# Performance work log

Hardware: AMD Instinct MI355X
Metric: run time of the kernel (lower is better)

Reference implementation:

```python
import jax, jax.numpy as jnp
import numpy as np

# dims: B=batch, S=src_len, H=hidden, E=char_embed, V=vocab, L=lstm layers
B, S, H, E, V, L = 512, 64, 1024, 256, 128, 2


def setup_inputs() -> dict:
    key = jax.random.key(0)
    ks = jax.random.split(key, 20)
    def n(k, shape, scale=0.05):
        return jax.random.normal(k, shape, dtype=jnp.float32) * scale
    return {
        "input_ids": jax.random.randint(ks[0], (B, 1), 0, V),
        "hidden": n(ks[1], (L, B, H), 1.0),
        "cell": n(ks[2], (L, B, H), 1.0),
        "encoder_outputs": n(ks[3], (B, S, H), 1.0),
        "emb": n(ks[4], (V, E)),          # nn.Embedding weight
        "U": n(ks[5], (H, H)),             # attention U (applied as x @ U)
        "W": n(ks[6], (H, H)),             # attention W
        "Vw": n(ks[7], (H, 1)),            # attention V -> scalar score
        "Wih0": n(ks[8], (4 * H, E + H)),  # LSTM layer0 input weights (i,f,g,o)
        "Whh0": n(ks[9], (4 * H, H)),
        "bih0": n(ks[10], (4 * H,)),
        "bhh0": n(ks[11], (4 * H,)),
        "Wih1": n(ks[12], (4 * H, H)),     # LSTM layer1
        "Whh1": n(ks[13], (4 * H, H)),
        "bih1": n(ks[14], (4 * H,)),
        "bhh1": n(ks[15], (4 * H,)),
        "out_w": n(ks[16], (V, H)),        # output nn.Linear weight (out,in)
        "out_b": n(ks[17], (V,)),
        "matrix": 0,
    }


def _lstm_step(x, h, c, Wih, Whh, bih, bhh):
    g = x @ Wih.T + h @ Whh.T + bih + bhh          # (B, 4H), torch gate order i,f,g,o
    i, f, gg, o = jnp.split(g, 4, axis=-1)
    c2 = jax.nn.sigmoid(f) * c + jax.nn.sigmoid(i) * jnp.tanh(gg)
    h2 = jax.nn.sigmoid(o) * jnp.tanh(c2)
    return h2, c2


def reference(input_ids, hidden, cell, encoder_outputs, emb, U, W, Vw,
              Wih0, Whh0, bih0, bhh0, Wih1, Whh1, bih1, bhh1,
              out_w, out_b, matrix):
    embedded = emb[input_ids]                                  # (B,1,E)
    t1 = jnp.einsum('bsh,hk->bsk', encoder_outputs, U)         # U(enc): (B,S,H)
    t2 = hidden[-1] @ W                                        # W(h_top): (B,H)
    e = jnp.tanh(t1 + t2[:, None, :]) @ Vw                     # scores: (B,S,1)
    a = jax.nn.softmax(e, axis=1)                              # attention weights over S
    ct = jnp.einsum('bso,bsh->boh', a, encoder_outputs)        # context: (B,1,H)
    x = jnp.concatenate([embedded, ct], axis=2)[:, 0, :]       # (B, E+H); dropout p=0 -> identity
    h0, c0 = _lstm_step(x, hidden[0], cell[0], Wih0, Whh0, bih0, bhh0)
    h1, c1 = _lstm_step(h0, hidden[1], cell[1], Wih1, Whh1, bih1, bhh1)
    out = (h1 @ out_w.T + out_b)[:, None, :]                   # (B,1,V)
    h_new = jnp.stack([h0, h1])
    c_new = jnp.stack([c0, c1])
    if matrix:
        return (a, out, h_new, c_new)
    return (out, h_new, c_new)
```

## Files before the change

kernel.cpp:

```cpp
#include <hip/hip_runtime.h>
#include <stdint.h>

#define BB 512
#define SS 64
#define HH 1024
#define EE 256
#define VV 128

typedef __attribute__((ext_vector_type(8))) short bf16x8;
typedef __attribute__((ext_vector_type(4))) float f32x4;
typedef __attribute__((ext_vector_type(8))) unsigned short u16x8;

constexpr size_t OFF_SCRATCH = 0;
constexpr size_t OFF_OUTW  = OFF_SCRATCH + 67108864UL;
constexpr size_t OFF_HID0  = OFF_OUTW  + 262144UL;
constexpr size_t OFF_HLAST = OFF_HID0  + 1048576UL;
constexpr size_t OFF_UT    = OFF_HLAST + 1048576UL;
constexpr size_t OFF_WT    = OFF_UT    + 2097152UL;
constexpr size_t OFF_T2    = OFF_WT    + 2097152UL;
constexpr size_t OFF_E     = OFF_T2    + 2097152UL;
constexpr size_t OFF_EMB   = OFF_E     + 131072UL;
constexpr size_t OFF_CT    = OFF_EMB   + 262144UL;
constexpr size_t OFF_G     = OFF_CT    + 1048576UL;
constexpr size_t OFF_H0B   = OFF_G     + 8388608UL;
constexpr size_t OFF_H1B   = OFF_H0B   + 1048576UL;

__device__ __forceinline__ unsigned short f2bf(float f) {
  unsigned int u = __float_as_uint(f);
  unsigned int r = (u + 0x7FFFu + ((u >> 16) & 1u)) >> 16;
  return (unsigned short)r;
}
__device__ __forceinline__ float bf2f(unsigned short h) {
  return __uint_as_float(((unsigned int)h) << 16);
}

__device__ __forceinline__ void gload_lds16(const void* g, void* l) {
  __builtin_amdgcn_global_load_lds(
      (const __attribute__((address_space(1))) unsigned int*)g,
      (__attribute__((address_space(3))) unsigned int*)l, 16, 0, 0);
}

__global__ __launch_bounds__(256) void cvt_small(const float* __restrict__ hid,
                                                 const float* __restrict__ outw,
                                                 char* __restrict__ ws) {
  int i = blockIdx.x * 256 + threadIdx.x;
  const float4* src;
  ushort4* dst;
  int j;
  if (i < 262144) { src = (const float4*)hid;  dst = (ushort4*)(ws + OFF_HID0); j = i; }
  else            { src = (const float4*)outw; dst = (ushort4*)(ws + OFF_OUTW); j = i - 262144; }
  float4 v = src[j];
  ushort4 o;
  o.x = f2bf(v.x); o.y = f2bf(v.y); o.z = f2bf(v.z); o.w = f2bf(v.w);
  dst[j] = o;
}

__global__ void transpose_cvt2(const float* __restrict__ U, const float* __restrict__ W,
                               char* __restrict__ ws) {
  __shared__ float tile[32][33];
  const float* in = blockIdx.z ? W : U;
  unsigned short* out = (unsigned short*)(ws + (blockIdx.z ? OFF_WT : OFF_UT));
  int bc = blockIdx.x * 32, br = blockIdx.y * 32;
  int tx = threadIdx.x & 31, ty = threadIdx.x >> 5;
#pragma unroll
  for (int i = 0; i < 32; i += 8)
    tile[ty + i][tx] = in[(long)(br + ty + i) * HH + bc + tx];
  __syncthreads();
#pragma unroll
  for (int i = 0; i < 32; i += 8)
    out[(long)(bc + ty + i) * HH + br + tx] = f2bf(tile[tx][ty + i]);
}

__global__ void build_xemb(const int* __restrict__ ids, const float* __restrict__ emb,
                           unsigned short* __restrict__ embb) {
  int t = blockIdx.x * 256 + threadIdx.x;
  int b = t >> 6, c4 = t & 63;
  float4 v = ((const float4*)(emb + (long)ids[b] * 256))[c4];
  ushort4 o;
  o.x = f2bf(v.x); o.y = f2bf(v.y); o.z = f2bf(v.z); o.w = f2bf(v.w);
  ((ushort4*)embb)[t] = o;
}

template <int BF32>
__global__ __launch_bounds__(256) void gemm_seg(
    const unsigned short* __restrict__ A0, int KA0,
    const unsigned short* __restrict__ A1, int KA1,
    const unsigned short* __restrict__ A2,
    const void* __restrict__ B0v, int KB0, const void* __restrict__ B1v,
    float* __restrict__ C0p, float* __restrict__ C1p, int N, int Ktot, int Khalf) {
  __shared__ alignas(128) unsigned short lA[128 * 64];
  __shared__ alignas(128) unsigned short lB[64 * 64];
  const int tid = threadIdx.x;
  const int lane = tid & 63, wid = tid >> 6;
  const int wr = wid >> 1, wc = wid & 1;
  const int fr = lane & 15, fg = lane >> 4;
  f32x4 acc[4][2] = {};
  const long rowA0 = (long)blockIdx.x * 128;
  const long rowB0 = (long)blockIdx.y * 64;
  const int ktb = blockIdx.z * Khalf;
  int kte = ktb + Khalf; if (kte > Ktot) kte = Ktot;
  float* C = blockIdx.z ? C1p : C0p;
  for (int kt = ktb; kt < kte; kt += 64) {
    const unsigned short* Ap; int ka, lda;
    if (kt < KA0)            { Ap = A0; ka = kt;             lda = KA0; }
    else if (kt < KA0 + KA1) { Ap = A1; ka = kt - KA0;       lda = KA1; }
    else                     { Ap = A2; ka = kt - KA0 - KA1; lda = 1024; }
    if constexpr (BF32) {
      const float* Bp; int kb, ldb;
      if (kt < KB0) { Bp = (const float*)B0v; kb = kt;       ldb = KB0; }
      else          { Bp = (const float*)B1v; kb = kt - KB0; ldb = 1024; }
      const int brow = tid >> 2, bkq = tid & 3;
      const f32x4* bs = (const f32x4*)(Bp + (rowB0 + brow) * (long)ldb + kb) + bkq * 4;
      f32x4 q0 = bs[0], q1 = bs[1], q2 = bs[2], q3 = bs[3];
#pragma unroll
      for (int j = 0; j < 4; ++j) {
        int c = j * 256 + tid;
        int r = c >> 3, cc = c & 7;
        int sc = cc ^ ((r >> 1) & 7);
        gload_lds16(Ap + (rowA0 + r) * (long)lda + ka + sc * 8, &lA[c * 8]);
      }
      const int bx = (brow >> 1) & 7;
      u16x8 w0, w1;
#pragma unroll
      for (int j = 0; j < 4; ++j) {
        w0[j] = f2bf(q0[j]); w0[4 + j] = f2bf(q1[j]);
        w1[j] = f2bf(q2[j]); w1[4 + j] = f2bf(q3[j]);
      }
      *(u16x8*)&lB[brow * 64 + (((bkq * 2) ^ bx) * 8)] = w0;
      *(u16x8*)&lB[brow * 64 + (((bkq * 2 + 1) ^ bx) * 8)] = w1;
    } else {
      const unsigned short* Bp; int kb, ldb;
      if (kt < KB0) { Bp = (const unsigned short*)B0v; kb = kt;       ldb = KB0; }
      else          { Bp = (const unsigned short*)B1v; kb = kt - KB0; ldb = 1024; }
#pragma unroll
      for (int j = 0; j < 4; ++j) {
        int c = j * 256 + tid;
        int r = c >> 3, cc = c & 7;
        int sc = cc ^ ((r >> 1) & 7);
        gload_lds16(Ap + (rowA0 + r) * (long)lda + ka + sc * 8, &lA[c * 8]);
      }
#pragma unroll
      for (int j = 0; j < 2; ++j) {
        int c = j * 256 + tid;
        int r = c >> 3, cc = c & 7;
        int sc = cc ^ ((r >> 1) & 7);
        gload_lds16(Bp + (rowB0 + r) * (long)ldb + kb + sc * 8, &lB[c * 8]);
      }
    }
    __syncthreads();
#pragma unroll
    for (int kk = 0; kk < 64; kk += 32) {
      bf16x8 af[4], bfv[2];
#pragma unroll
      for (int m = 0; m < 4; ++m) {
        int row = wr * 64 + m * 16 + fr;
        int ch = ((kk >> 3) + fg) ^ ((row >> 1) & 7);
        af[m] = *(const bf16x8*)&lA[row * 64 + ch * 8];
      }
#pragma unroll
      for (int n = 0; n < 2; ++n) {
        int row = wc * 32 + n * 16 + fr;
        int ch = ((kk >> 3) + fg) ^ ((row >> 1) & 7);
        bfv[n] = *(const bf16x8*)&lB[row * 64 + ch * 8];
      }
#pragma unroll
      for (int m = 0; m < 4; ++m)
#pragma unroll
        for (int n = 0; n < 2; ++n)
          acc[m][n] = __builtin_amdgcn_mfma_f32_16x16x32_bf16(af[m], bfv[n],
                                                              acc[m][n], 0, 0, 0);
    }
    __syncthreads();
  }
#pragma unroll
  for (int m = 0; m < 4; ++m)
#pragma unroll
    for (int n = 0; n < 2; ++n)
#pragma unroll
      for (int r = 0; r < 4; ++r) {
        long grow = rowA0 + wr * 64 + m * 16 + fg * 4 + r;
        long gcol = rowB0 + wc * 32 + n * 16 + fr;
        C[grow * N + gcol] = acc[m][n][r];
      }
}

__global__ __launch_bounds__(256) void gemm_outproj(
    const unsigned short* __restrict__ A, const unsigned short* __restrict__ Bt,
    float* __restrict__ C) {
  __shared__ alignas(128) unsigned short lA[128 * 64];
  __shared__ alignas(128) unsigned short lB[128 * 64];
  const int tid = threadIdx.x;
  const int lane = tid & 63, wid = tid >> 6;
  const int wr = wid >> 1, wc = wid & 1;
  const int fr = lane & 15, fg = lane >> 4;
  f32x4 acc[4][4] = {};
  const long rowA0 = (long)blockIdx.x * 128;
  const int k0 = blockIdx.y * 128;
  for (int kt = k0; kt < k0 + 128; kt += 64) {
#pragma unroll
    for (int j = 0; j < 4; ++j) {
      int c = j * 256 + tid;
      int r = c >> 3, cc = c & 7;
      gload_lds16(A + (rowA0 + r) * 1024 + kt + cc * 8, &lA[c * 8]);
    }
#pragma unroll
    for (int j = 0; j < 4; ++j) {
      int c = j * 256 + tid;
      int r = c >> 3, cc = c & 7;
      gload_lds16(Bt + (long)r * 1024 + kt + cc * 8, &lB[c * 8]);
    }
    __syncthreads();
#pragma unroll
    for (int kk = 0; kk < 64; kk += 32) {
      bf16x8 af[4], bfv[4];
#pragma unroll
      for (int m = 0; m < 4; ++m)
        af[m] = *(const bf16x8*)&lA[(wr * 64 + m * 16 + fr) * 64 + kk + fg * 8];
#pragma unroll
      for (int n = 0; n < 4; ++n)
        bfv[n] = *(const bf16x8*)&lB[(wc * 64 + n * 16 + fr) * 64 + kk + fg * 8];
#pragma unroll
      for (int m = 0; m < 4; ++m)
#pragma unroll
        for (int n = 0; n < 4; ++n)
          acc[m][n] = __builtin_amdgcn_mfma_f32_16x16x32_bf16(af[m], bfv[n],
                                                              acc[m][n], 0, 0, 0);
    }
    __syncthreads();
  }
#pragma unroll
  for (int m = 0; m < 4; ++m)
#pragma unroll
    for (int n = 0; n < 4; ++n)
#pragma unroll
      for (int r = 0; r < 4; ++r) {
        long grow = rowA0 + wr * 64 + m * 16 + fg * 4 + r;
        long gcol = wc * 64 + n * 16 + fr;
        atomicAdd(&C[grow * 128 + gcol], acc[m][n][r]);
      }
}

__global__ void init_out_bias(const float* __restrict__ ob, float* __restrict__ out) {
  int i = blockIdx.x * 256 + threadIdx.x;
  out[i] = ob[i & 127];
}

__global__ __launch_bounds__(512, 2) void gemm_score128(
    const float* __restrict__ Af, const unsigned short* __restrict__ Bt,
    const float* __restrict__ t2, const float* __restrict__ Vw,
    float* __restrict__ e) {
  extern __shared__ unsigned short smem[];
  const int tid = threadIdx.x;
  const int lane = tid & 63, wid = tid >> 6;
  const int wr = wid >> 2;
  const int wcc = wid & 3;
  const int fr = lane & 15, fg = lane >> 4;
  int flat = blockIdx.y * 4 + blockIdx.x;
  int swz = (flat & 7) * 128 + (flat >> 3);
  const long rowA0 = (long)(swz >> 2) * 128;
  const long rowB0 = (long)(swz & 3) * 256;

  f32x4 acc[4][4] = {};

  const int arow = tid >> 2, akq = tid & 3;
  const int akh = akq >> 1, ach = akq & 1;
  const float* ag = Af + (rowA0 + arow) * 1024 + akq * 16;
  const int awx = (arow >> 1) & 3;
  f32x4 areg[4];

  auto issueA = [&](int kt) {
    const f32x4* p = (const f32x4*)(ag + kt * 64);
#pragma unroll
    for (int j = 0; j < 4; ++j) areg[j] = p[j];
  };
  auto writeA = [&](int buf) {
    unsigned short* wb = smem + buf * 24576 + akh * 4096 + arow * 32;
#pragma unroll
    for (int w = 0; w < 2; ++w) {
      u16x8 o;
#pragma unroll
      for (int q = 0; q < 8; ++q) o[q] = f2bf(areg[w * 2 + (q >> 2)][q & 3]);
      *(u16x8*)(wb + (((ach * 2 + w) ^ awx) * 8)) = o;
    }
  };
  auto stageB = [&](int buf, int kt) {
#pragma unroll
    for (int kh = 0; kh < 2; ++kh) {
      unsigned short* dst = smem + buf * 24576 + 8192 + kh * 8192;
      int kb = kt * 64 + kh * 32;
#pragma unroll
      for (int j = 0; j < 2; ++j) {
        int c = j * 512 + tid;
        int row = c >> 2;
        int fgl = (c & 3) ^ ((row >> 1) & 3);
        gload_lds16(Bt + (rowB0 + row) * 1024L + kb + fgl * 8, dst + c * 8);
      }
    }
  };
  auto readA4 = [&](int buf, int kh, bf16x8* af) {
    const unsigned short* rg = smem + buf * 24576 + kh * 4096;
#pragma unroll
    for (int m = 0; m < 4; ++m) {
      int row = wr * 64 + m * 16 + fr;
      int slot = fg ^ ((row >> 1) & 3);
      af[m] = *(const bf16x8*)(rg + row * 32 + slot * 8);
    }
  };
  auto readB4 = [&](int buf, int kh, bf16x8* bv) {
    const unsigned short* rg = smem + buf * 24576 + 8192 + kh * 8192;
#pragma unroll
    for (int n = 0; n < 4; ++n) {
      int row = wcc * 64 + n * 16 + fr;
      int slot = fg ^ ((row >> 1) & 3);
      bv[n] = *(const bf16x8*)(rg + row * 32 + slot * 8);
    }
  };
  auto mfma16 = [&](const bf16x8* af, const bf16x8* bv) {
    __builtin_amdgcn_s_setprio(1);
#pragma unroll
    for (int m = 0; m < 4; ++m)
#pragma unroll
      for (int n = 0; n < 4; ++n)
        acc[m][n] = __builtin_amdgcn_mfma_f32_16x16x32_bf16(af[m], bv[n],
                                                            acc[m][n], 0, 0, 0);
    __builtin_amdgcn_s_setprio(0);
  };

  issueA(0);
  stageB(0, 0);
  asm volatile("s_waitcnt vmcnt(4)" ::: "memory");
  writeA(0);
  issueA(1);
  asm volatile("s_waitcnt lgkmcnt(0)" ::: "memory");
  asm volatile("s_waitcnt vmcnt(4)" ::: "memory");
  __builtin_amdgcn_s_barrier();
  __builtin_amdgcn_sched_barrier(0);

#pragma unroll 2
  for (int u = 0; u < 16; ++u) {
    const int cur = u & 1, nxt = cur ^ 1;
    stageB(nxt, (u + 1) & 15);
    bf16x8 af[4], bv[4];
    readB4(cur, 0, bv);
    readA4(cur, 0, af);
    mfma16(af, bv);
    writeA(nxt);
    issueA((u + 2) & 15);
    readB4(cur, 1, bv);
    readA4(cur, 1, af);
    asm volatile("s_waitcnt lgkmcnt(0)" ::: "memory");
    __builtin_amdgcn_sched_barrier(0);
    mfma16(af, bv);
    asm volatile("s_waitcnt vmcnt(4)" ::: "memory");
    __builtin_amdgcn_s_barrier();
    __builtin_amdgcn_sched_barrier(0);
  }
  asm volatile("s_waitcnt vmcnt(0)" ::: "memory");

  const long bidx = (rowA0 >> 6) + wr;
  float t2v[4], vw[4];
#pragma unroll
  for (int n = 0; n < 4; ++n) {
    long col = rowB0 + wcc * 64 + n * 16 + fr;
    vw[n] = Vw[col];
    t2v[n] = t2[bidx * HH + col];
  }
#pragma unroll
  for (int i = 0; i < 4; ++i) {
    float part[4] = {0.f, 0.f, 0.f, 0.f};
#pragma unroll
    for (int n = 0; n < 4; ++n) {
#pragma unroll
      for (int r = 0; r < 4; ++r) {
        float tval = acc[i][n][r] + t2v[n];
        float th = 1.f - 2.f / (__expf(2.f * tval) + 1.f);
        part[r] += th * vw[n];
      }
    }
#pragma unroll
    for (int r = 0; r < 4; ++r) {
      float p = part[r];
      p += __shfl_xor(p, 1);
      p += __shfl_xor(p, 2);
      p += __shfl_xor(p, 4);
      p += __shfl_xor(p, 8);
      if (fr == 0)
        atomicAdd(&e[rowA0 + wr * 64 + i * 16 + fg * 4 + r], p);
    }
  }
}

__global__ void softmax_ctx(const float* __restrict__ e,
                            const float* __restrict__ enc,
                            unsigned short* __restrict__ ctb) {
  __shared__ float als[2][64];
  const int tid = threadIdx.x;
  const int bpair = blockIdx.x;
  if (tid < 128) {
    int b = bpair * 2 + (tid >> 6), s = tid & 63;
    float v = e[b * 64 + s];
    float mx = v;
#pragma unroll
    for (int o = 32; o; o >>= 1) mx = fmaxf(mx, __shfl_xor(mx, o));
    float ex = __expf(v - mx);
    float sm = ex;
#pragma unroll
    for (int o = 32; o; o >>= 1) sm += __shfl_xor(sm, o);
    als[tid >> 6][s] = ex / sm;
  }
  __syncthreads();
  int bi = tid >> 7, hg = tid & 127;
  int b = bpair * 2 + bi;
  const float* er = enc + (long)b * (SS * HH) + hg * 8;
  float s[8] = {0.f, 0.f, 0.f, 0.f, 0.f, 0.f, 0.f, 0.f};
  for (int i = 0; i < 64; ++i) {
    float av = als[bi][i];
    f32x4 v0 = *(const f32x4*)(er + (long)i * HH);
    f32x4 v1 = *(const f32x4*)(er + (long)i * HH + 4);
#pragma unroll
    for (int j = 0; j < 4; ++j) { s[j] += av * v0[j]; s[4 + j] += av * v1[j]; }
  }
  unsigned short* dst = ctb + (long)b * HH + hg * 8;
#pragma unroll
  for (int j = 0; j < 8; ++j) dst[j] = f2bf(s[j]);
}

__global__ void lstm_cell(const float* __restrict__ g0, const float* __restrict__ g1,
                          const float* __restrict__ bih, const float* __restrict__ bhh,
                          const float* __restrict__ cin,
                          float* __restrict__ hout, float* __restrict__ cout,
                          unsigned short* __restrict__ hb) {
  int idx = blockIdx.x * 256 + threadIdx.x;
  int b = idx >> 10, h = idx & 1023;
  const float* gr0 = g0 + (long)b * 4096;
  const float* gr1 = g1 + (long)b * 4096;
  float gi = gr0[h] + gr1[h] + bih[h] + bhh[h];
  float gf = gr0[1024 + h] + gr1[1024 + h] + bih[1024 + h] + bhh[1024 + h];
  float gg = gr0[2048 + h] + gr1[2048 + h] + bih[2048 + h] + bhh[2048 + h];
  float go = gr0[3072 + h] + gr1[3072 + h] + bih[3072 + h] + bhh[3072 + h];
  float si = 1.f / (1.f + __expf(-gi));
  float sf = 1.f / (1.f + __expf(-gf));
  float so = 1.f / (1.f + __expf(-go));
  float tg = 1.f - 2.f / (__expf(2.f * gg) + 1.f);
  float c2 = sf * cin[idx] + si * tg;
  float tc = 1.f - 2.f / (__expf(2.f * c2) + 1.f);
  float h2 = so * tc;
  cout[idx] = c2;
  hout[idx] = h2;
  hb[idx] = f2bf(h2);
}

extern "C" void kernel_launch(void* const* d_in, const int* in_sizes, int n_in,
                              void* d_out, int out_size, void* d_ws, size_t ws_size,
                              hipStream_t stream) {
  const int* ids = (const int*)d_in[0];
  const float* hidden = (const float*)d_in[1];
  const float* cell = (const float*)d_in[2];
  const float* enc = (const float*)d_in[3];
  const float* emb = (const float*)d_in[4];
  const float* U = (const float*)d_in[5];
  const float* W = (const float*)d_in[6];
  const float* Vw = (const float*)d_in[7];
  const float* Wih0 = (const float*)d_in[8];
  const float* Whh0 = (const float*)d_in[9];
  const float* bih0 = (const float*)d_in[10];
  const float* bhh0 = (const float*)d_in[11];
  const float* Wih1 = (const float*)d_in[12];
  const float* Whh1 = (const float*)d_in[13];
  const float* bih1 = (const float*)d_in[14];
  const float* bhh1 = (const float*)d_in[15];
  const float* out_w = (const float*)d_in[16];
  const float* out_b = (const float*)d_in[17];
  float* out = (float*)d_out;
  char* ws = (char*)d_ws;
  (void)in_sizes; (void)n_in; (void)out_size; (void)ws_size;

  unsigned short* outwb  = (unsigned short*)(ws + OFF_OUTW);
  unsigned short* hid0b  = (unsigned short*)(ws + OFF_HID0);
  unsigned short* hlastb = (unsigned short*)(ws + OFF_HLAST);
  unsigned short* Utb    = (unsigned short*)(ws + OFF_UT);
  unsigned short* Wtb    = (unsigned short*)(ws + OFF_WT);
  float*          t2     = (float*)(ws + OFF_T2);
  float*          e      = (float*)(ws + OFF_E);
  unsigned short* embb   = (unsigned short*)(ws + OFF_EMB);
  unsigned short* ctb    = (unsigned short*)(ws + OFF_CT);
  float*          g      = (float*)(ws + OFF_G);
  float*          gB     = (float*)(ws + OFF_SCRATCH);
  unsigned short* h0b    = (unsigned short*)(ws + OFF_H0B);
  unsigned short* h1b    = (unsigned short*)(ws + OFF_H1B);

  float* out_logits = out;
  float* h_new = out + BB * VV;
  float* c_new = h_new + 2 * BB * HH;

  cvt_small<<<1152, 256, 0, stream>>>(hidden, out_w, ws);
  transpose_cvt2<<<dim3(32, 32, 2), 256, 0, stream>>>(U, W, ws);
  build_xemb<<<128, 256, 0, stream>>>(ids, emb, embb);
  hipMemsetAsync(e, 0, (size_t)BB * SS * 4, stream);

  gemm_seg<0><<<dim3(4, 16, 1), 256, 0, stream>>>(hlastb, 1024, nullptr, 0, nullptr,
                                                  Wtb, 1024, nullptr, t2, t2, HH, 1024, 1024);

  (void)hipFuncSetAttribute(reinterpret_cast<const void*>(gemm_score128),
                            hipFuncAttributeMaxDynamicSharedMemorySize, 98304);
  gemm_score128<<<dim3(4, 256), 512, 98304, stream>>>(enc, Utb, t2, Vw, e);

  softmax_ctx<<<256, 256, 0, stream>>>(e, enc, ctb);

  gemm_seg<1><<<dim3(4, 64, 2), 256, 0, stream>>>(embb, 256, ctb, 1024, hid0b,
                                                  Wih0, 1280, Whh0, g, gB, 4 * HH, 2304, 1152);
  lstm_cell<<<BB * HH / 256, 256, 0, stream>>>(g, gB, bih0, bhh0, cell, h_new, c_new, h0b);

  gemm_seg<1><<<dim3(4, 64, 2), 256, 0, stream>>>(h0b, 1024, hlastb, 1024, nullptr,
                                                  Wih1, 1024, Whh1, g, gB, 4 * HH, 2048, 1024);
  lstm_cell<<<BB * HH / 256, 256, 0, stream>>>(g, gB, bih1, bhh1, cell + BB * HH,
                                               h_new + BB * HH, c_new + BB * HH, h1b);

  init_out_bias<<<BB * VV / 256, 256, 0, stream>>>(out_b, out_logits);
  gemm_outproj<<<dim3(4, 8), 256, 0, stream>>>(h1b, outwb, out_logits);
}
```

Baseline: 260.6 us.

## Replace pipelined score GEMM with simpler 128x128-tile single-buffer kernel and fast bf16 packing

Rewrites the attention score GEMM from a 512-thread, 128x256-tile, double-buffered, software-pipelined kernel with dynamic shared memory into a 256-thread, 128x128-tile kernel that uses static shared memory and a plain load, sync, compute loop. It also swaps the round-to-nearest fp32-to-bf16 conversion for a byte-permute truncation (pkbf) in both the score GEMM and the gemm_seg fp32 B path. The smaller tiles and lower LDS use should allow more resident blocks, and the conversion uses fewer instructions. In exchange the explicit load/compute overlap is lost, the grid doubles so A is reloaded more often, and truncating instead of rounding adds slight bias to the bf16 values.

```diff
diff --git a/kernel.cpp b/kernel.cpp
--- a/kernel.cpp
+++ b/kernel.cpp
@@ -32,6 +32,9 @@
 }
 __device__ __forceinline__ float bf2f(unsigned short h) {
   return __uint_as_float(((unsigned int)h) << 16);
+}
+__device__ __forceinline__ unsigned int pkbf(float a, float b) {
+  return __builtin_amdgcn_perm(__float_as_uint(b), __float_as_uint(a), 0x07060302u);
 }
 
 __device__ __forceinline__ void gload_lds16(const void* g, void* l) {
@@ -120,14 +123,13 @@
         gload_lds16(Ap + (rowA0 + r) * (long)lda + ka + sc * 8, &lA[c * 8]);
       }
       const int bx = (brow >> 1) & 7;
-      u16x8 w0, w1;
-#pragma unroll
-      for (int j = 0; j < 4; ++j) {
-        w0[j] = f2bf(q0[j]); w0[4 + j] = f2bf(q1[j]);
-        w1[j] = f2bf(q2[j]); w1[4 + j] = f2bf(q3[j]);
-      }
-      *(u16x8*)&lB[brow * 64 + (((bkq * 2) ^ bx) * 8)] = w0;
-      *(u16x8*)&lB[brow * 64 + (((bkq * 2 + 1) ^ bx) * 8)] = w1;
+      uint4 w0, w1;
+      w0.x = pkbf(q0[0], q0[1]); w0.y = pkbf(q0[2], q0[3]);
+      w0.z = pkbf(q1[0], q1[1]); w0.w = pkbf(q1[2], q1[3]);
+      w1.x = pkbf(q2[0], q2[1]); w1.y = pkbf(q2[2], q2[3]);
+      w1.z = pkbf(q3[0], q3[1]); w1.w = pkbf(q3[2], q3[3]);
+      *(uint4*)&lB[brow * 64 + (((bkq * 2) ^ bx) * 8)] = w0;
+      *(uint4*)&lB[brow * 64 + (((bkq * 2 + 1) ^ bx) * 8)] = w1;
     } else {
       const unsigned short* Bp; int kb, ldb;
       if (kt < KB0) { Bp = (const unsigned short*)B0v; kb = kt;       ldb = KB0; }
@@ -245,123 +247,89 @@
   out[i] = ob[i & 127];
 }
 
-__global__ __launch_bounds__(512, 2) void gemm_score128(
+__global__ __launch_bounds__(256) void gemm_score128f(
     const float* __restrict__ Af, const unsigned short* __restrict__ Bt,
     const float* __restrict__ t2, const float* __restrict__ Vw,
     float* __restrict__ e) {
-  extern __shared__ unsigned short smem[];
+  __shared__ alignas(128) unsigned short lA[8192];
+  __shared__ alignas(128) unsigned short lB[8192];
   const int tid = threadIdx.x;
   const int lane = tid & 63, wid = tid >> 6;
-  const int wr = wid >> 2;
-  const int wcc = wid & 3;
+  const int wr = wid >> 1, wc = wid & 1;
   const int fr = lane & 15, fg = lane >> 4;
-  int flat = blockIdx.y * 4 + blockIdx.x;
-  int swz = (flat & 7) * 128 + (flat >> 3);
-  const long rowA0 = (long)(swz >> 2) * 128;
-  const long rowB0 = (long)(swz & 3) * 256;
+  int flat = blockIdx.y * 8 + blockIdx.x;
+  int swz = (flat & 7) * 256 + (flat >> 3);
+  const long rowA0 = (long)(swz >> 3) * 128;
+  const long rowB0 = (long)(swz & 7) * 128;
 
   f32x4 acc[4][4] = {};
 
-  const int arow = tid >> 2, akq = tid & 3;
-  const int akh = akq >> 1, ach = akq & 1;
-  const float* ag = Af + (rowA0 + arow) * 1024 + akq * 16;
+  const int arow = tid >> 1, akh = tid & 1;
+  const float* ag = Af + (rowA0 + arow) * 1024 + akh * 32;
   const int awx = (arow >> 1) & 3;
-  f32x4 areg[4];
-
-  auto issueA = [&](int kt) {
-    const f32x4* p = (const f32x4*)(ag + kt * 64);
-#pragma unroll
-    for (int j = 0; j < 4; ++j) areg[j] = p[j];
-  };
-  auto writeA = [&](int buf) {
-    unsigned short* wb = smem + buf * 24576 + akh * 4096 + arow * 32;
-#pragma unroll
-    for (int w = 0; w < 2; ++w) {
-      u16x8 o;
-#pragma unroll
-      for (int q = 0; q < 8; ++q) o[q] = f2bf(areg[w * 2 + (q >> 2)][q & 3]);
-      *(u16x8*)(wb + (((ach * 2 + w) ^ awx) * 8)) = o;
-    }
-  };
-  auto stageB = [&](int buf, int kt) {
-#pragma unroll
-    for (int kh = 0; kh < 2; ++kh) {
-      unsigned short* dst = smem + buf * 24576 + 8192 + kh * 8192;
-      int kb = kt * 64 + kh * 32;
-#pragma unroll
-      for (int j = 0; j < 2; ++j) {
-        int c = j * 512 + tid;
-        int row = c >> 2;
-        int fgl = (c & 3) ^ ((row >> 1) & 3);
-        gload_lds16(Bt + (rowB0 + row) * 1024L + kb + fgl * 8, dst + c * 8);
-      }
-    }
-  };
-  auto readA4 = [&](int buf, int kh, bf16x8* af) {
-    const unsigned short* rg = smem + buf * 24576 + kh * 4096;
-#pragma unroll
-    for (int m = 0; m < 4; ++m) {
-      int row = wr * 64 + m * 16 + fr;
-      int slot = fg ^ ((row >> 1) & 3);
-      af[m] = *(const bf16x8*)(rg + row * 32 + slot * 8);
-    }
-  };
-  auto readB4 = [&](int buf, int kh, bf16x8* bv) {
-    const unsigned short* rg = smem + buf * 24576 + 8192 + kh * 8192;
-#pragma unroll
-    for (int n = 0; n < 4; ++n) {
-      int row = wcc * 64 + n * 16 + fr;
-      int slot = fg ^ ((row >> 1) & 3);
-      bv[n] = *(const bf16x8*)(rg + row * 32 + slot * 8);
-    }
-  };
-  auto mfma16 = [&](const bf16x8* af, const bf16x8* bv) {
-    __builtin_amdgcn_s_setprio(1);
-#pragma unroll
-    for (int m = 0; m < 4; ++m)
-#pragma unroll
-      for (int n = 0; n < 4; ++n)
-        acc[m][n] = __builtin_amdgcn_mfma_f32_16x16x32_bf16(af[m], bv[n],
-                                                            acc[m][n], 0, 0, 0);
-    __builtin_amdgcn_s_setprio(0);
-  };
-
-  issueA(0);
-  stageB(0, 0);
-  asm volatile("s_waitcnt vmcnt(4)" ::: "memory");
-  writeA(0);
-  issueA(1);
-  asm volatile("s_waitcnt lgkmcnt(0)" ::: "memory");
-  asm volatile("s_waitcnt vmcnt(4)" ::: "memory");
-  __builtin_amdgcn_s_barrier();
-  __builtin_amdgcn_sched_barrier(0);
-
-#pragma unroll 2
-  for (int u = 0; u < 16; ++u) {
-    const int cur = u & 1, nxt = cur ^ 1;
-    stageB(nxt, (u + 1) & 15);
-    bf16x8 af[4], bv[4];
-    readB4(cur, 0, bv);
-    readA4(cur, 0, af);
-    mfma16(af, bv);
-    writeA(nxt);
-    issueA((u + 2) & 15);
-    readB4(cur, 1, bv);
-    readA4(cur, 1, af);
-    asm volatile("s_waitcnt lgkmcnt(0)" ::: "memory");
-    __builtin_amdgcn_sched_barrier(0);
-    mfma16(af, bv);
-    asm volatile("s_waitcnt vmcnt(4)" ::: "memory");
-    __builtin_amdgcn_s_barrier();
-    __builtin_amdgcn_sched_barrier(0);
-  }
-  asm volatile("s_waitcnt vmcnt(0)" ::: "memory");
+  unsigned short* awb = lA + akh * 4096 + arow * 32;
+
+  for (int kt = 0; kt < 16; ++kt) {
+#pragma unroll
+    for (int j = 0; j < 4; ++j) {
+      int c = j * 256 + tid;
+      int r = c >> 3, cc = c & 7;
+      int sc = cc ^ ((r >> 1) & 7);
+      gload_lds16(Bt + (rowB0 + r) * 1024L + kt * 64 + sc * 8, &lB[c * 8]);
+    }
+    const f32x4* ap = (const f32x4*)(ag + kt * 64);
+    {
+      f32x4 q0 = ap[0], q1 = ap[1], q2 = ap[2], q3 = ap[3];
+      uint4 w0, w1;
+      w0.x = pkbf(q0[0], q0[1]); w0.y = pkbf(q0[2], q0[3]);
+      w0.z = pkbf(q1[0], q1[1]); w0.w = pkbf(q1[2], q1[3]);
+      w1.x = pkbf(q2[0], q2[1]); w1.y = pkbf(q2[2], q2[3]);
+      w1.z = pkbf(q3[0], q3[1]); w1.w = pkbf(q3[2], q3[3]);
+      *(uint4*)(awb + (((0 ^ awx ^ akh) & 3) * 8)) = w0;
+      *(uint4*)(awb + (((1 ^ awx ^ akh) & 3) * 8)) = w1;
+    }
+    {
+      f32x4 q0 = ap[4], q1 = ap[5], q2 = ap[6], q3 = ap[7];
+      uint4 w0, w1;
+      w0.x = pkbf(q0[0], q0[1]); w0.y = pkbf(q0[2], q0[3]);
+      w0.z = pkbf(q1[0], q1[1]); w0.w = pkbf(q1[2], q1[3]);
+      w1.x = pkbf(q2[0], q2[1]); w1.y = pkbf(q2[2], q2[3]);
+      w1.z = pkbf(q3[0], q3[1]); w1.w = pkbf(q3[2], q3[3]);
+      *(uint4*)(awb + (((2 ^ awx ^ akh) & 3) * 8)) = w0;
+      *(uint4*)(awb + (((3 ^ awx ^ akh) & 3) * 8)) = w1;
+    }
+    __syncthreads();
+#pragma unroll
+    for (int kk = 0; kk < 64; kk += 32) {
+      const int kh = kk >> 5;
+      bf16x8 af[4], bv[4];
+#pragma unroll
+      for (int m = 0; m < 4; ++m) {
+        int row = wr * 64 + m * 16 + fr;
+        int slot = (fg ^ ((row >> 1) & 3) ^ kh) & 3;
+        af[m] = *(const bf16x8*)&lA[kh * 4096 + row * 32 + slot * 8];
+      }
+#pragma unroll
+      for (int n = 0; n < 4; ++n) {
+        int row = wc * 64 + n * 16 + fr;
+        int ch = ((kk >> 3) + fg) ^ ((row >> 1) & 7);
+        bv[n] = *(const bf16x8*)&lB[row * 64 + ch * 8];
+      }
+#pragma unroll
+      for (int m = 0; m < 4; ++m)
+#pragma unroll
+        for (int n = 0; n < 4; ++n)
+          acc[m][n] = __builtin_amdgcn_mfma_f32_16x16x32_bf16(af[m], bv[n],
+                                                              acc[m][n], 0, 0, 0);
+    }
+    __syncthreads();
+  }
 
   const long bidx = (rowA0 >> 6) + wr;
   float t2v[4], vw[4];
 #pragma unroll
   for (int n = 0; n < 4; ++n) {
-    long col = rowB0 + wcc * 64 + n * 16 + fr;
+    long col = rowB0 + wc * 64 + n * 16 + fr;
     vw[n] = Vw[col];
     t2v[n] = t2[bidx * HH + col];
   }
@@ -501,9 +469,7 @@
   gemm_seg<0><<<dim3(4, 16, 1), 256, 0, stream>>>(hlastb, 1024, nullptr, 0, nullptr,
                                                   Wtb, 1024, nullptr, t2, t2, HH, 1024, 1024);
 
-  (void)hipFuncSetAttribute(reinterpret_cast<const void*>(gemm_score128),
-                            hipFuncAttributeMaxDynamicSharedMemorySize, 98304);
-  gemm_score128<<<dim3(4, 256), 512, 98304, stream>>>(enc, Utb, t2, Vw, e);
+  gemm_score128f<<<dim3(8, 256), 256, 0, stream>>>(enc, Utb, t2, Vw, e);
 
   softmax_ctx<<<256, 256, 0, stream>>>(e, enc, ctb);
 
```

New measurement: 321.0 us. 1.23x slower.
